# Optimization experiments

Hardware: AMD Instinct MI355X
Metric: run time of the kernel (lower is better)

The kernel has to match this reference:

```python
import jax, jax.numpy as jnp
import numpy as np

B, N, C = 2, 2048, 768
H, HD = 12, 64
HID = 3072
LN_EPS = 1e-5
POL_EPS = 1e-6


def _layer_norm(x, g, b):
    m = jnp.mean(x, axis=-1, keepdims=True)
    v = jnp.mean(jnp.square(x - m), axis=-1, keepdims=True)
    return (x - m) * jax.lax.rsqrt(v + LN_EPS) * g + b


def _softmax_with_policy(attn, policy):
    # attn: [B,H,N,N], policy: [B,N,1]
    n = attn.shape[-1]
    ap = policy.reshape(policy.shape[0], 1, 1, n)  # [B,1,1,N]
    eye = jnp.eye(n, dtype=ap.dtype)[None, None]   # [1,1,N,N]
    ap = ap + (1.0 - ap) * eye                     # always attend to self
    attn = attn - jnp.max(attn, axis=-1, keepdims=True)
    attn = jnp.exp(attn.astype(jnp.float32)) * ap.astype(jnp.float32)
    attn = (attn + POL_EPS / n) / (jnp.sum(attn, axis=-1, keepdims=True) + POL_EPS)
    return attn


def setup_inputs() -> dict:
    key = jax.random.key(0)
    ks = jax.random.split(key, 12)
    s = lambda fan_in: 1.0 / np.sqrt(fan_in)
    x = jax.random.normal(ks[0], (B, N, C), dtype=jnp.float32)
    policy = (jax.random.uniform(ks[1], (B, N, 1)) > 0.5).astype(jnp.float32)
    return {
        "x": x,
        "policy": policy,
        "ln1_g": jnp.ones((C,), jnp.float32),
        "ln1_b": jnp.zeros((C,), jnp.float32),
        "qkv_w": jax.random.uniform(ks[2], (3 * H * HD, C), jnp.float32, -s(C), s(C)),
        "proj_w": jax.random.uniform(ks[3], (C, H * HD), jnp.float32, -s(H * HD), s(H * HD)),
        "proj_b": jnp.zeros((C,), jnp.float32),
        "ln2_g": jnp.ones((C,), jnp.float32),
        "ln2_b": jnp.zeros((C,), jnp.float32),
        "fc1_w": jax.random.uniform(ks[4], (HID, C), jnp.float32, -s(C), s(C)),
        "fc1_b": jnp.zeros((HID,), jnp.float32),
        "fc2_w": jax.random.uniform(ks[5], (C, HID), jnp.float32, -s(HID), s(HID)),
        "fc2_b": jnp.zeros((C,), jnp.float32),
    }


def reference(x, policy, ln1_g, ln1_b, qkv_w, proj_w, proj_b, ln2_g, ln2_b, fc1_w, fc1_b, fc2_w, fc2_b):
    b, n, c = x.shape
    scale = HD ** -0.5
    # --- attention branch (pre-LN) ---
    h = _layer_norm(x, ln1_g, ln1_b)
    qkv = (h @ qkv_w.T).reshape(b, n, 3, H, HD).transpose(2, 0, 3, 1, 4)  # [3,B,H,N,hd]
    q, k, v = qkv[0], qkv[1], qkv[2]
    attn = jnp.einsum("bhqd,bhkd->bhqk", q * scale, k)
    attn = _softmax_with_policy(attn, policy).astype(x.dtype)
    o = jnp.einsum("bhqk,bhkd->bhqd", attn, v).transpose(0, 2, 1, 3).reshape(b, n, H * HD)
    x = x + (o @ proj_w.T + proj_b)  # skip_lam = 1.0, dropout/drop_path = identity
    # --- MLP branch (pre-LN) ---
    h = _layer_norm(x, ln2_g, ln2_b)
    h = jax.nn.gelu(h @ fc1_w.T + fc1_b, approximate=False)  # torch nn.GELU = exact erf
    x = x + (h @ fc2_w.T + fc2_b)
    return x
```

## Files before the change

kernel.cpp:

```cpp
#include <hip/hip_runtime.h>

typedef unsigned short u16;
typedef unsigned int u32;
typedef float f32x4 __attribute__((ext_vector_type(4)));
typedef float f32x16 __attribute__((ext_vector_type(16)));
typedef __bf16 bf16x8 __attribute__((ext_vector_type(8)));
typedef u16 u16x4v __attribute__((ext_vector_type(4)));
typedef u32 u32x2 __attribute__((ext_vector_type(2)));
typedef u32 u32x4 __attribute__((ext_vector_type(4)));

#define NHEAD 12
#define NN 2048
#define CC 768

#define GLOBAL_AS __attribute__((address_space(1)))
#define LDS_AS __attribute__((address_space(3)))

__device__ __forceinline__ u16 tobf(float f) {
  __bf16 h = (__bf16)f;
  return __builtin_bit_cast(u16, h);
}
__device__ __forceinline__ float bf2f(u16 h) {
  u32 u = ((u32)h) << 16;
  return __builtin_bit_cast(float, u);
}
__device__ __forceinline__ u32 cvtpk(float lo, float hi) {
  u32 r;
  asm("v_cvt_pk_bf16_f32 %0, %1, %2" : "=v"(r) : "v"(lo), "v"(hi));
  return r;
}
__device__ __forceinline__ void plswap(u32& a, u32& b) {
  asm volatile("v_permlane32_swap_b32 %0, %1" : "+v"(a), "+v"(b));
}
__device__ __forceinline__ void plswapf(float& a, float& b) {
  asm volatile("v_permlane32_swap_b32 %0, %1" : "+v"(a), "+v"(b));
}

#define N4_QKV 442368
#define N4_PROJ 147456
#define N4_FC 589824
__global__ __launch_bounds__(256) void cvt4_kernel(
    const float* __restrict__ a, const float* __restrict__ b,
    const float* __restrict__ c, const float* __restrict__ d,
    u16* __restrict__ oa, u16* __restrict__ ob, u16* __restrict__ oc,
    u16* __restrict__ od) {
  int i = blockIdx.x * 256 + threadIdx.x;
  const float* src;
  u16* dst;
  if (i < N4_QKV) {
    src = a; dst = oa;
  } else if (i < N4_QKV + N4_PROJ) {
    i -= N4_QKV; src = b; dst = ob;
  } else if (i < N4_QKV + N4_PROJ + N4_FC) {
    i -= N4_QKV + N4_PROJ; src = c; dst = oc;
  } else {
    i -= N4_QKV + N4_PROJ + N4_FC; src = d; dst = od;
    if (i >= N4_FC) return;
  }
  float4 v = ((const float4*)src)[i];
  u16x4v o = {tobf(v.x), tobf(v.y), tobf(v.z), tobf(v.w)};
  ((u16x4v*)dst)[i] = o;
}

__global__ __launch_bounds__(256) void ln_kernel(const float* __restrict__ x,
                                                 const float* __restrict__ gw,
                                                 const float* __restrict__ bw,
                                                 u16* __restrict__ out) {
  int row = blockIdx.x * 4 + (threadIdx.x >> 6);
  int lane = threadIdx.x & 63;
  const float* xr = x + (size_t)row * CC + lane * 12;
  float v[12];
  *(float4*)&v[0] = *(const float4*)(xr + 0);
  *(float4*)&v[4] = *(const float4*)(xr + 4);
  *(float4*)&v[8] = *(const float4*)(xr + 8);
  float s = 0.f, sq = 0.f;
#pragma unroll
  for (int j = 0; j < 12; ++j) { s += v[j]; sq += v[j] * v[j]; }
#pragma unroll
  for (int o = 1; o < 64; o <<= 1) { s += __shfl_xor(s, o); sq += __shfl_xor(sq, o); }
  float mean = s * (1.f / CC);
  float var = sq * (1.f / CC) - mean * mean;
  float rs = rsqrtf(var + 1e-5f);
  u16 ob[12];
#pragma unroll
  for (int j = 0; j < 12; ++j) {
    int c = lane * 12 + j;
    ob[j] = tobf((v[j] - mean) * rs * gw[c] + bw[c]);
  }
  u32* orow = (u32*)(out + (size_t)row * CC + lane * 12);
#pragma unroll
  for (int j = 0; j < 6; ++j) orow[j] = (u32)ob[2 * j] | ((u32)ob[2 * j + 1] << 16);
}

template <int BM, int OB, int HASB, int ACT, int RES>
__global__ __launch_bounds__(256) void gemm_kernel(
    const u16* __restrict__ A, const u16* __restrict__ Bw,
    const float* __restrict__ bias, const float* __restrict__ res,
    void* __restrict__ Cout, int M, int N, int K) {
  constexpr int MW = BM / 2;
  constexpr int MF = MW / 16;
  __shared__ __align__(16) u16 Alds[BM * 64];
  __shared__ __align__(16) u16 Blds[128 * 64];
  const int tid = threadIdx.x;
  const int lane = tid & 63, wave = tid >> 6;
  const int l15 = lane & 15, g = lane >> 4;
  const int nx = gridDim.x;
  const int flat = blockIdx.y * nx + blockIdx.x;
  const int cpx = (nx * gridDim.y) >> 3;
  const int swz = (flat & 7) * cpx + (flat >> 3);
  const int bm = (swz % nx) * BM, bn = (swz / nx) * 128;
  const int wm = (wave >> 1) * MW, wn = (wave & 1) * 64;
  f32x4 acc[MF][4] = {};

  for (int kt = 0; kt < K; kt += 64) {
#pragma unroll
    for (int i = 0; i < BM / 32; ++i) {
      int ob_ = i * 4096 + wave * 1024;
      int lb = ob_ + lane * 16;
      int row = lb >> 7;
      int cb = (lb & 127) ^ ((row & 7) << 4);
      const u16* sa = A + (size_t)(bm + row) * K + kt + (cb >> 1);
      __builtin_amdgcn_global_load_lds((const GLOBAL_AS void*)sa,
                                       (LDS_AS void*)(Alds + (ob_ >> 1)), 16, 0, 0);
    }
#pragma unroll
    for (int i = 0; i < 4; ++i) {
      int ob_ = i * 4096 + wave * 1024;
      int lb = ob_ + lane * 16;
      int row = lb >> 7;
      int cb = (lb & 127) ^ ((row & 7) << 4);
      const u16* sb = Bw + (size_t)(bn + row) * K + kt + (cb >> 1);
      __builtin_amdgcn_global_load_lds((const GLOBAL_AS void*)sb,
                                       (LDS_AS void*)(Blds + (ob_ >> 1)), 16, 0, 0);
    }
    __syncthreads();
#pragma unroll
    for (int ks = 0; ks < 2; ++ks) {
      bf16x8 af[MF], bfr[4];
#pragma unroll
      for (int mi = 0; mi < MF; ++mi) {
        int row = wm + mi * 16 + l15;
        int cb = (ks * 64 + g * 16) ^ ((row & 7) << 4);
        af[mi] = *(const bf16x8*)&Alds[row * 64 + (cb >> 1)];
      }
#pragma unroll
      for (int ni = 0; ni < 4; ++ni) {
        int row = wn + ni * 16 + l15;
        int cb = (ks * 64 + g * 16) ^ ((row & 7) << 4);
        bfr[ni] = *(const bf16x8*)&Blds[row * 64 + (cb >> 1)];
      }
#pragma unroll
      for (int mi = 0; mi < MF; ++mi)
#pragma unroll
        for (int ni = 0; ni < 4; ++ni)
          acc[mi][ni] = __builtin_amdgcn_mfma_f32_16x16x32_bf16(af[mi], bfr[ni],
                                                                acc[mi][ni], 0, 0, 0);
    }
    __syncthreads();
  }
#pragma unroll
  for (int mi = 0; mi < MF; ++mi) {
#pragma unroll
    for (int ni = 0; ni < 4; ++ni) {
      int col = bn + wn + ni * 16 + l15;
      float bs = HASB ? bias[col] : 0.f;
#pragma unroll
      for (int r = 0; r < 4; ++r) {
        int rowm = bm + wm + mi * 16 + g * 4 + r;
        float v = acc[mi][ni][r] + bs;
        if (ACT) v = 0.5f * v * (1.f + erff(v * 0.70710678118654752f));
        if (RES) v += res[(size_t)rowm * N + col];
        if (OB)
          ((u16*)Cout)[(size_t)rowm * N + col] = tobf(v);
        else
          ((float*)Cout)[(size_t)rowm * N + col] = v;
      }
    }
  }
}

__global__ __launch_bounds__(256) void vsum_kernel(const u16* __restrict__ qkv,
                                                   float* __restrict__ vs) {
  int bh = blockIdx.x, q4 = blockIdx.y;
  int b = bh / NHEAD, h = bh % NHEAD;
  int d = threadIdx.x & 63, part = threadIdx.x >> 6;
  float s = 0.f;
  for (int n = q4 * 512 + part; n < q4 * 512 + 512; n += 4)
    s += bf2f(qkv[(size_t)(b * NN + n) * 2304 + 2 * CC + h * 64 + d]);
  __shared__ float red[256];
  red[threadIdx.x] = s;
  __syncthreads();
  if (threadIdx.x < 64) {
    float t = red[threadIdx.x] + red[threadIdx.x + 64] + red[threadIdx.x + 128] +
              red[threadIdx.x + 192];
    vs[q4 * (24 * 64) + bh * 64 + threadIdx.x] = t;
  }
}

#define SCL2E 0.18033688f
#define TRRD(dst, addr, OFF) \
  asm volatile("ds_read_b64_tr_b16 %0, %1 offset:" OFF : "=v"(dst) : "v"(addr))

__global__ __launch_bounds__(256) void attn32_kernel(const u16* __restrict__ qkv,
                                                     const float* __restrict__ policy,
                                                     float* __restrict__ partO,
                                                     float* __restrict__ partlm) {
  __shared__ __align__(16) u16 Klds[2][4096];
  __shared__ __align__(16) u16 Vlds[2][4096];
  __shared__ float PolF[NN];
  __shared__ float alf[4][32];
  const int bh = blockIdx.y, b = bh / NHEAD, h = bh % NHEAD;
  const int qt = blockIdx.x >> 1, half = blockIdx.x & 1;
  const int tid = threadIdx.x, lane = tid & 63, w = tid >> 6;
  const int l31 = lane & 31, hp = lane >> 5, b4 = (lane >> 4) & 1;
  const int q0 = qt * 128 + w * 32;
  const int dv = q0 >> 6;
  const int ktd = (q0 >> 5) & 1;
  const int kv0 = half * 1024;
  const size_t adv = (size_t)64 * 2304;

  bf16x8 qf0, qf1, qf2, qf3;
  {
    const u16* qp = qkv + (size_t)(b * NN + q0 + l31) * 2304 + h * 64 + 8 * hp;
#pragma unroll
    for (int ds = 0; ds < 4; ++ds) {
      bf16x8 r = *(const bf16x8*)(qp + ds * 16);
      bf16x8 o;
#pragma unroll
      for (int j = 0; j < 8; ++j) o[j] = (__bf16)((float)r[j] * SCL2E);
      if (ds == 0) qf0 = o; else if (ds == 1) qf1 = o; else if (ds == 2) qf2 = o; else qf3 = o;
    }
  }

  const u16* ksrc[2];
  const u16* vsrcp[2];
#pragma unroll
  for (int c = 0; c < 2; ++c) {
    int lb = c * 4096 + w * 1024 + lane * 16;
    int row = lb >> 7;
    int cb = (lb & 127) ^ ((row & 7) << 4);
    ksrc[c] = qkv + (size_t)(b * NN + kv0 + row) * 2304 + CC + h * 64 + (cb >> 1);
    int idx0 = (c * 256 + w * 64 + lane) * 8;
    int s0 = idx0 & 15, jj = (idx0 >> 4) & 3, b4v = (idx0 >> 6) & 1,
        pv = (idx0 >> 7) & 1, hv = (idx0 >> 8) & 1, dtv = (idx0 >> 9) & 1,
        mkv = (idx0 >> 10) & 3;
    int key = mkv * 16 + 8 * hv + 4 * pv + jj;
    int d0 = dtv * 32 + 16 * b4v + s0;
    vsrcp[c] = qkv + (size_t)(b * NN + kv0 + key) * 2304 + 2 * CC + h * 64 + d0;
  }
  auto stage = [&](int buf) {
#pragma unroll
    for (int c = 0; c < 2; ++c) {
      __builtin_amdgcn_global_load_lds((const GLOBAL_AS void*)ksrc[c],
                                       (LDS_AS void*)&Klds[buf][c * 2048 + w * 512], 16, 0, 0);
      __builtin_amdgcn_global_load_lds((const GLOBAL_AS void*)vsrcp[c],
                                       (LDS_AS void*)&Vlds[buf][c * 2048 + w * 512], 16, 0, 0);
      ksrc[c] += adv; vsrcp[c] += adv;
    }
  };

  stage(0);
  {
    float4 p0 = *(const float4*)&policy[b * NN + tid * 8];
    float4 p1 = *(const float4*)&policy[b * NN + tid * 8 + 4];
    *(float4*)&PolF[tid * 8] = p0;
    *(float4*)&PolF[tid * 8 + 4] = p1;
  }
  __syncthreads();

  float m_cur = -3.0e38f, m_true = -3.0e38f, l_run = 0.f;
  f32x16 accd[2] = {};
  const u32 vbase = (u32)(uintptr_t)(LDS_AS u16*)&Vlds[0][0] +
                    (u32)(2 * (lane & 15) + 128 * b4 + 512 * hp);

#pragma unroll 1
  for (int t = 0; t < 16; ++t) {
    const int cur = t & 1;
    const int kvg = kv0 + t * 64;
    if (t < 15) stage(cur ^ 1);

    f32x16 sv0, sv1;
    {
      bf16x8 kf[4];
#pragma unroll
      for (int ds = 0; ds < 4; ++ds) {
        int row = l31;
        int cb = (32 * ds + 16 * hp) ^ ((row & 7) << 4);
        kf[ds] = *(const bf16x8*)((const char*)&Klds[cur][0] + row * 128 + cb);
      }
      f32x16 a = {};
      a = __builtin_amdgcn_mfma_f32_32x32x16_bf16(kf[0], qf0, a, 0, 0, 0);
      a = __builtin_amdgcn_mfma_f32_32x32x16_bf16(kf[1], qf1, a, 0, 0, 0);
      a = __builtin_amdgcn_mfma_f32_32x32x16_bf16(kf[2], qf2, a, 0, 0, 0);
      a = __builtin_amdgcn_mfma_f32_32x32x16_bf16(kf[3], qf3, a, 0, 0, 0);
      sv0 = a;
    }
    {
      bf16x8 kf[4];
#pragma unroll
      for (int ds = 0; ds < 4; ++ds) {
        int row = 32 + l31;
        int cb = (32 * ds + 16 * hp) ^ ((row & 7) << 4);
        kf[ds] = *(const bf16x8*)((const char*)&Klds[cur][0] + row * 128 + cb);
      }
      f32x16 a = {};
      a = __builtin_amdgcn_mfma_f32_32x32x16_bf16(kf[0], qf0, a, 0, 0, 0);
      a = __builtin_amdgcn_mfma_f32_32x32x16_bf16(kf[1], qf1, a, 0, 0, 0);
      a = __builtin_amdgcn_mfma_f32_32x32x16_bf16(kf[2], qf2, a, 0, 0, 0);
      a = __builtin_amdgcn_mfma_f32_32x32x16_bf16(kf[3], qf3, a, 0, 0, 0);
      sv1 = a;
    }

    u32x2 tr[4][2][2];
    {
      u32 vab = vbase + (u32)(cur * 8192);
      TRRD(tr[0][0][0], vab, "0");    TRRD(tr[0][0][1], vab, "256");
      TRRD(tr[0][1][0], vab, "1024"); TRRD(tr[0][1][1], vab, "1280");
      TRRD(tr[1][0][0], vab, "2048"); TRRD(tr[1][0][1], vab, "2304");
      TRRD(tr[1][1][0], vab, "3072"); TRRD(tr[1][1][1], vab, "3328");
      TRRD(tr[2][0][0], vab, "4096"); TRRD(tr[2][0][1], vab, "4352");
      TRRD(tr[3][0][0], vab, "6144"); TRRD(tr[3][0][1], vab, "6400");
      TRRD(tr[2][1][0], vab, "5120"); TRRD(tr[2][1][1], vab, "5376");
      TRRD(tr[3][1][0], vab, "7168"); TRRD(tr[3][1][1], vab, "7424");
    }

    float ta = fmaxf(fmaxf(sv0[0], sv0[1]), sv0[2]);
    float tb = fmaxf(fmaxf(sv0[3], sv0[4]), sv0[5]);
    float tc = fmaxf(fmaxf(sv0[6], sv0[7]), sv0[8]);
    float td = fmaxf(fmaxf(sv0[9], sv0[10]), sv0[11]);
    float te = fmaxf(fmaxf(sv0[12], sv0[13]), sv0[14]);
    float tf = fmaxf(fmaxf(sv0[15], sv1[0]), sv1[1]);
    float tg = fmaxf(fmaxf(sv1[2], sv1[3]), sv1[4]);
    float th = fmaxf(fmaxf(sv1[5], sv1[6]), sv1[7]);
    float ti = fmaxf(fmaxf(sv1[8], sv1[9]), sv1[10]);
    float tj = fmaxf(fmaxf(sv1[11], sv1[12]), sv1[13]);
    float tk = fmaxf(sv1[14], sv1[15]);
    float tmax = fmaxf(fmaxf(fmaxf(fmaxf(ta, tb), fmaxf(tc, td)),
                             fmaxf(fmaxf(te, tf), fmaxf(tg, th))),
                       fmaxf(fmaxf(ti, tj), tk));
    {
      float t1 = tmax, t2 = tmax;
      plswapf(t1, t2);
      tmax = fmaxf(t1, t2);
    }
    m_true = fmaxf(m_true, tmax);
    const bool defer = __all(tmax <= m_cur + 8.f);
    const float m_new = defer ? m_cur : fmaxf(m_cur, tmax);

    const bool isdiag = ((half * 16 + t) == dv);
    float ev[32];
#pragma unroll
    for (int kt = 0; kt < 2; ++kt) {
#pragma unroll
      for (int i = 0; i < 4; ++i) {
        float4 pq = *(const float4*)&PolF[kvg + kt * 32 + 8 * i + 4 * hp];
#pragma unroll
        for (int rq = 0; rq < 4; ++rq) {
          int r = 4 * i + rq;
          float ap = ((const float*)&pq)[rq];
          if (isdiag && kt == ktd) ap = ((8 * i + 4 * hp + rq) == l31) ? 1.f : ap;
          float sval = kt ? sv1[r] : sv0[r];
          ev[kt * 16 + r] = __builtin_amdgcn_exp2f(sval - m_new) * ap;
        }
      }
    }
    u32 wv[16];
#pragma unroll
    for (int j = 0; j < 16; ++j) wv[j] = cvtpk(ev[2 * j], ev[2 * j + 1]);
    float ps[16];
#pragma unroll
    for (int j = 0; j < 16; ++j)
      ps[j] = __builtin_bit_cast(float, wv[j] << 16) +
              __builtin_bit_cast(float, wv[j] & 0xffff0000u);
#pragma unroll
    for (int s = 8; s > 0; s >>= 1)
#pragma unroll
      for (int j = 0; j < s; ++j) ps[j] += ps[j + s];
    float psum = ps[0];
    {
      float s1 = psum, s2 = psum;
      plswapf(s1, s2);
      psum = s1 + s2;
    }
    if (!defer) {
      float alpha = __builtin_amdgcn_exp2f(m_cur - m_new);
      l_run = l_run * alpha + psum;
      m_cur = m_new;
      if (lane < 32) alf[w][lane] = alpha;
      float4 aq0 = *(const float4*)&alf[w][4 * hp];
      float4 aq1 = *(const float4*)&alf[w][8 + 4 * hp];
      float4 aq2 = *(const float4*)&alf[w][16 + 4 * hp];
      float4 aq3 = *(const float4*)&alf[w][24 + 4 * hp];
#pragma unroll
      for (int dt = 0; dt < 2; ++dt) {
#pragma unroll
        for (int rq = 0; rq < 4; ++rq) {
          accd[dt][0 + rq] *= ((const float*)&aq0)[rq];
          accd[dt][4 + rq] *= ((const float*)&aq1)[rq];
          accd[dt][8 + rq] *= ((const float*)&aq2)[rq];
          accd[dt][12 + rq] *= ((const float*)&aq3)[rq];
        }
      }
    } else {
      l_run += psum;
    }

    u32 PK[4][4];
#pragma unroll
    for (int mk = 0; mk < 4; ++mk) {
      int bw_ = 8 * (mk >> 1) + 4 * (mk & 1);
      PK[mk][0] = wv[bw_ + 0];
      PK[mk][1] = wv[bw_ + 1];
      PK[mk][2] = wv[bw_ + 2];
      PK[mk][3] = wv[bw_ + 3];
      plswap(PK[mk][2], PK[mk][0]);
      plswap(PK[mk][3], PK[mk][1]);
    }

    asm volatile("s_waitcnt lgkmcnt(0)" ::: "memory");
    __builtin_amdgcn_sched_barrier(0);

#pragma unroll
    for (int mk = 0; mk < 4; ++mk) {
      u32x4 pk4 = {PK[mk][0], PK[mk][1], PK[mk][2], PK[mk][3]};
      bf16x8 pf = __builtin_bit_cast(bf16x8, pk4);
#pragma unroll
      for (int dt = 0; dt < 2; ++dt) {
        u32x4 vv = {tr[mk][dt][0].x, tr[mk][dt][0].y, tr[mk][dt][1].x, tr[mk][dt][1].y};
        bf16x8 vf = __builtin_bit_cast(bf16x8, vv);
        accd[dt] = __builtin_amdgcn_mfma_f32_32x32x16_bf16(pf, vf, accd[dt], 0, 0, 0);
      }
    }
    __syncthreads();
  }

  float sr = __builtin_amdgcn_exp2f(m_cur - m_true);
  if (lane < 32) {
    alf[w][lane] = sr;
    float2 lm = {l_run * sr, m_true};
    *(float2*)&partlm[2 * ((size_t)(half * 24 + bh) * 2048 + q0 + lane)] = lm;
  }
  float4 sq0 = *(const float4*)&alf[w][4 * hp];
  float4 sq1 = *(const float4*)&alf[w][8 + 4 * hp];
  float4 sq2 = *(const float4*)&alf[w][16 + 4 * hp];
  float4 sq3 = *(const float4*)&alf[w][24 + 4 * hp];
  float* pb2 = partO + ((size_t)(half * 24 + bh) * 2048) * 64;
#pragma unroll
  for (int dt = 0; dt < 2; ++dt) {
#pragma unroll
    for (int i = 0; i < 4; ++i) {
      float4 sqv = (i == 0) ? sq0 : (i == 1) ? sq1 : (i == 2) ? sq2 : sq3;
#pragma unroll
      for (int rq = 0; rq < 4; ++rq) {
        int row = q0 + 8 * i + 4 * hp + rq;
        pb2[(size_t)row * 64 + dt * 32 + l31] = accd[dt][4 * i + rq] * ((const float*)&sqv)[rq];
      }
    }
  }
}

__global__ __launch_bounds__(256) void merge_kernel(const float* __restrict__ partO,
                                                    const float* __restrict__ partlm,
                                                    const float* __restrict__ vs,
                                                    u16* __restrict__ o) {
  int rr = blockIdx.x * 4 + (threadIdx.x >> 6);
  int lane = threadIdx.x & 63;
  int bh = rr >> 11, q = rr & 2047;
  int b = bh / NHEAD, h = bh % NHEAD;
  const float* O1 = partO + ((size_t)bh * 2048 + q) * 64;
  const float* O2 = partO + ((size_t)(24 + bh) * 2048 + q) * 64;
  float2 lm1 = ((const float2*)partlm)[(size_t)bh * 2048 + q];
  float2 lm2 = ((const float2*)partlm)[(size_t)(24 + bh) * 2048 + q];
  float ms = fmaxf(lm1.y, lm2.y);
  float w1 = exp2f(lm1.y - ms), w2 = exp2f(lm2.y - ms);
  float den = lm1.x * w1 + lm2.x * w2 + 1e-6f;
  float vsv = vs[bh * 64 + lane] + vs[1536 + bh * 64 + lane] +
              vs[3072 + bh * 64 + lane] + vs[4608 + bh * 64 + lane];
  float num = O1[lane] * w1 + O2[lane] * w2 + (1e-6f / 2048.f) * vsv;
  o[((size_t)(b * NN + q)) * CC + h * 64 + lane] = tobf(num / den);
}

extern "C" void kernel_launch(void* const* d_in, const int* in_sizes, int n_in,
                              void* d_out, int out_size, void* d_ws, size_t ws_size,
                              hipStream_t stream) {
  const float* x = (const float*)d_in[0];
  const float* policy = (const float*)d_in[1];
  const float* ln1g = (const float*)d_in[2];
  const float* ln1b = (const float*)d_in[3];
  const float* qkvw = (const float*)d_in[4];
  const float* projw = (const float*)d_in[5];
  const float* projb = (const float*)d_in[6];
  const float* ln2g = (const float*)d_in[7];
  const float* ln2b = (const float*)d_in[8];
  const float* fc1w = (const float*)d_in[9];
  const float* fc1b = (const float*)d_in[10];
  const float* fc2w = (const float*)d_in[11];
  const float* fc2b = (const float*)d_in[12];
  float* out = (float*)d_out;

  char* ws = (char*)d_ws;
  size_t off = 0;
  auto alloc = [&](size_t bytes) {
    void* p = ws + off;
    off = (off + bytes + 255) & ~(size_t)255;
    return p;
  };
  u16* wq = (u16*)alloc((size_t)2304 * 768 * 2);
  u16* wp = (u16*)alloc((size_t)768 * 768 * 2);
  u16* w1 = (u16*)alloc((size_t)3072 * 768 * 2);
  u16* w2 = (u16*)alloc((size_t)768 * 3072 * 2);
  u16* hbuf = (u16*)alloc((size_t)4096 * 768 * 2);
  u16* qkv = (u16*)alloc((size_t)4096 * 2304 * 2);
  u16* obuf = (u16*)alloc((size_t)4096 * 768 * 2);
  float* vs = (float*)alloc((size_t)4 * 24 * 64 * 4);
  size_t unionOff = off;
  float* partO = (float*)alloc((size_t)2 * 24 * 2048 * 64 * 4);
  float* partlm = (float*)alloc((size_t)2 * 24 * 2048 * 2 * 4);
  float* x1 = (float*)(ws + unionOff);
  u16* f1 = qkv;

  cvt4_kernel<<<6912, 256, 0, stream>>>(qkvw, projw, fc1w, fc2w, wq, wp, w1, w2);

  ln_kernel<<<1024, 256, 0, stream>>>(x, ln1g, ln1b, hbuf);
  gemm_kernel<128, 1, 0, 0, 0><<<dim3(32, 18), 256, 0, stream>>>(
      hbuf, wq, nullptr, nullptr, qkv, 4096, 2304, 768);
  vsum_kernel<<<dim3(24, 4), 256, 0, stream>>>(qkv, vs);
  attn32_kernel<<<dim3(32, 24), 256, 0, stream>>>(qkv, policy, partO, partlm);
  merge_kernel<<<12288, 256, 0, stream>>>(partO, partlm, vs, obuf);
  gemm_kernel<64, 0, 1, 0, 1><<<dim3(64, 6), 256, 0, stream>>>(
      obuf, wp, projb, x, x1, 4096, 768, 768);
  ln_kernel<<<1024, 256, 0, stream>>>(x1, ln2g, ln2b, hbuf);
  gemm_kernel<128, 1, 1, 1, 0><<<dim3(32, 24), 256, 0, stream>>>(
      hbuf, w1, fc1b, nullptr, f1, 4096, 3072, 768);
  gemm_kernel<64, 0, 1, 0, 1><<<dim3(64, 6), 256, 0, stream>>>(
      f1, w2, fc2b, x1, out, 4096, 768, 3072);
}
```

Before: 248.2 us.

## Compact keys/values to policy-active tokens and handle self-attention term in merge

Result: faster. 232.0 us (-6.6%).

```diff
diff --git a/kernel.cpp b/kernel.cpp
--- a/kernel.cpp
+++ b/kernel.cpp
@@ -197,27 +197,75 @@
   }
 }
 
+__global__ __launch_bounds__(256) void scan_kernel(const float* __restrict__ policy,
+                                                   int* __restrict__ ncbuf,
+                                                   int* __restrict__ idxbuf) {
+  int b = blockIdx.x, tid = threadIdx.x;
+  float pv[8];
+  *(float4*)&pv[0] = *(const float4*)&policy[b * NN + tid * 8];
+  *(float4*)&pv[4] = *(const float4*)&policy[b * NN + tid * 8 + 4];
+  int cnt = 0;
+#pragma unroll
+  for (int j = 0; j < 8; ++j) cnt += (pv[j] != 0.f) ? 1 : 0;
+  __shared__ int sc[256];
+  sc[tid] = cnt;
+  __syncthreads();
+  for (int off = 1; off < 256; off <<= 1) {
+    int v = sc[tid];
+    int add = (tid >= off) ? sc[tid - off] : 0;
+    __syncthreads();
+    sc[tid] = v + add;
+    __syncthreads();
+  }
+  int base = sc[tid] - cnt;
+#pragma unroll
+  for (int j = 0; j < 8; ++j) {
+    if (pv[j] != 0.f) idxbuf[b * NN + base++] = tid * 8 + j;
+  }
+  if (tid == 255) ncbuf[b] = sc[255];
+}
+
+__global__ __launch_bounds__(256) void gather_kernel(const u16* __restrict__ qkv,
+                                                     const int* __restrict__ ncbuf,
+                                                     const int* __restrict__ idxbuf,
+                                                     u16* __restrict__ ckv) {
+  int b = blockIdx.y;
+  int nc = ncbuf[b];
+  int ncp = (nc + 127) & ~127;
+  int c = blockIdx.x * 256 + threadIdx.x;
+  int j = c / 192, col = (c % 192) * 8;
+  if (j >= ncp) return;
+  uint4 val = {0, 0, 0, 0};
+  if (j < nc) {
+    int src = idxbuf[b * NN + j];
+    val = *(const uint4*)&qkv[(size_t)(b * NN + src) * 2304 + CC + col];
+  }
+  *(uint4*)&ckv[(size_t)(b * NN + j) * 1536 + col] = val;
+}
+
 #define SCL2E 0.18033688f
 #define TRRD(dst, addr, OFF) \
   asm volatile("ds_read_b64_tr_b16 %0, %1 offset:" OFF : "=v"(dst) : "v"(addr))
 
 __global__ __launch_bounds__(256) void attn32_kernel(const u16* __restrict__ qkv,
-                                                     const float* __restrict__ policy,
+                                                     const u16* __restrict__ ckv,
+                                                     const int* __restrict__ ncbuf,
                                                      float* __restrict__ partO,
                                                      float* __restrict__ partlm) {
   __shared__ __align__(16) u16 Klds[2][4096];
   __shared__ __align__(16) u16 Vlds[2][4096];
-  __shared__ float PolF[NN];
   __shared__ float alf[4][32];
   const int bh = blockIdx.y, b = bh / NHEAD, h = bh % NHEAD;
   const int qt = blockIdx.x >> 1, half = blockIdx.x & 1;
   const int tid = threadIdx.x, lane = tid & 63, w = tid >> 6;
   const int l31 = lane & 31, hp = lane >> 5, b4 = (lane >> 4) & 1;
   const int q0 = qt * 128 + w * 32;
-  const int dv = q0 >> 6;
-  const int ktd = (q0 >> 5) & 1;
-  const int kv0 = half * 1024;
-  const size_t adv = (size_t)64 * 2304;
+  const int nc = ncbuf[b];
+  const int ncp = (nc + 127) & ~127;
+  const int nh = ncp >> 1;
+  const int nt = nh >> 6;
+  const int kv0 = half * nh;
+  const size_t adv = (size_t)64 * 1536;
 
   bf16x8 qf0, qf1, qf2, qf3;
   {
@@ -239,14 +287,14 @@
     int lb = c * 4096 + w * 1024 + lane * 16;
     int row = lb >> 7;
     int cb = (lb & 127) ^ ((row & 7) << 4);
-    ksrc[c] = qkv + (size_t)(b * NN + kv0 + row) * 2304 + CC + h * 64 + (cb >> 1);
+    ksrc[c] = ckv + (size_t)(b * NN + kv0 + row) * 1536 + h * 64 + (cb >> 1);
     int idx0 = (c * 256 + w * 64 + lane) * 8;
     int s0 = idx0 & 15, jj = (idx0 >> 4) & 3, b4v = (idx0 >> 6) & 1,
         pv = (idx0 >> 7) & 1, hv = (idx0 >> 8) & 1, dtv = (idx0 >> 9) & 1,
         mkv = (idx0 >> 10) & 3;
     int key = mkv * 16 + 8 * hv + 4 * pv + jj;
     int d0 = dtv * 32 + 16 * b4v + s0;
-    vsrcp[c] = qkv + (size_t)(b * NN + kv0 + key) * 2304 + 2 * CC + h * 64 + d0;
+    vsrcp[c] = ckv + (size_t)(b * NN + kv0 + key) * 1536 + CC + h * 64 + d0;
   }
   auto stage = [&](int buf) {
 #pragma unroll
@@ -260,12 +308,6 @@
   };
 
   stage(0);
-  {
-    float4 p0 = *(const float4*)&policy[b * NN + tid * 8];
-    float4 p1 = *(const float4*)&policy[b * NN + tid * 8 + 4];
-    *(float4*)&PolF[tid * 8] = p0;
-    *(float4*)&PolF[tid * 8 + 4] = p1;
-  }
   __syncthreads();
 
   float m_cur = -3.0e38f, m_true = -3.0e38f, l_run = 0.f;
@@ -274,10 +316,9 @@
                     (u32)(2 * (lane & 15) + 128 * b4 + 512 * hp);
 
 #pragma unroll 1
-  for (int t = 0; t < 16; ++t) {
+  for (int t = 0; t < nt; ++t) {
     const int cur = t & 1;
-    const int kvg = kv0 + t * 64;
-    if (t < 15) stage(cur ^ 1);
+    if (t < nt - 1) stage(cur ^ 1);
 
     f32x16 sv0, sv1;
     {
@@ -347,20 +388,19 @@
     const bool defer = __all(tmax <= m_cur + 8.f);
     const float m_new = defer ? m_cur : fmaxf(m_cur, tmax);
 
-    const bool isdiag = ((half * 16 + t) == dv);
+    const int thr = nc - (kv0 + t * 64);
     float ev[32];
 #pragma unroll
     for (int kt = 0; kt < 2; ++kt) {
 #pragma unroll
       for (int i = 0; i < 4; ++i) {
-        float4 pq = *(const float4*)&PolF[kvg + kt * 32 + 8 * i + 4 * hp];
 #pragma unroll
         for (int rq = 0; rq < 4; ++rq) {
           int r = 4 * i + rq;
-          float ap = ((const float*)&pq)[rq];
-          if (isdiag && kt == ktd) ap = ((8 * i + 4 * hp + rq) == l31) ? 1.f : ap;
+          int kidx = kt * 32 + 8 * i + 4 * hp + rq;
           float sval = kt ? sv1[r] : sv0[r];
-          ev[kt * 16 + r] = __builtin_amdgcn_exp2f(sval - m_new) * ap;
+          float e = __builtin_amdgcn_exp2f(sval - m_new);
+          ev[kt * 16 + r] = (kidx < thr) ? e : 0.f;
         }
       }
     }
@@ -462,6 +502,8 @@
 __global__ __launch_bounds__(256) void merge_kernel(const float* __restrict__ partO,
                                                     const float* __restrict__ partlm,
                                                     const float* __restrict__ vs,
+                                                    const float* __restrict__ policy,
+                                                    const u16* __restrict__ qkv,
                                                     u16* __restrict__ o) {
   int rr = blockIdx.x * 4 + (threadIdx.x >> 6);
   int lane = threadIdx.x & 63;
@@ -473,10 +515,23 @@
   float2 lm2 = ((const float2*)partlm)[(size_t)(24 + bh) * 2048 + q];
   float ms = fmaxf(lm1.y, lm2.y);
   float w1 = exp2f(lm1.y - ms), w2 = exp2f(lm2.y - ms);
-  float den = lm1.x * w1 + lm2.x * w2 + 1e-6f;
+  float num_d = 0.f, den_d = 0.f;
+  if (policy[b * NN + q] == 0.f) {
+    const u16* rowp = qkv + (size_t)(b * NN + q) * 2304 + h * 64 + lane;
+    float qd = bf2f(rowp[0]);
+    float kd = bf2f(rowp[CC]);
+    float vv = bf2f(rowp[2 * CC]);
+    float dp = qd * kd;
+#pragma unroll
+    for (int of = 1; of < 64; of <<= 1) dp += __shfl_xor(dp, of);
+    float e = exp2f(dp * 0.18033688f - ms);
+    num_d = e * vv;
+    den_d = e;
+  }
+  float den = lm1.x * w1 + lm2.x * w2 + den_d + 1e-6f;
   float vsv = vs[bh * 64 + lane] + vs[1536 + bh * 64 + lane] +
               vs[3072 + bh * 64 + lane] + vs[4608 + bh * 64 + lane];
-  float num = O1[lane] * w1 + O2[lane] * w2 + (1e-6f / 2048.f) * vsv;
+  float num = O1[lane] * w1 + O2[lane] * w2 + num_d + (1e-6f / 2048.f) * vsv;
   o[((size_t)(b * NN + q)) * CC + h * 64 + lane] = tobf(num / den);
 }
 
@@ -510,14 +565,17 @@
   u16* w1 = (u16*)alloc((size_t)3072 * 768 * 2);
   u16* w2 = (u16*)alloc((size_t)768 * 3072 * 2);
   u16* hbuf = (u16*)alloc((size_t)4096 * 768 * 2);
+  u16* obuf = (u16*)alloc((size_t)4096 * 768 * 2);
   u16* qkv = (u16*)alloc((size_t)4096 * 2304 * 2);
-  u16* obuf = (u16*)alloc((size_t)4096 * 768 * 2);
   float* vs = (float*)alloc((size_t)4 * 24 * 64 * 4);
+  int* ncbuf = (int*)alloc(2 * sizeof(int));
+  int* idxbuf = (int*)alloc((size_t)2 * NN * sizeof(int));
   size_t unionOff = off;
   float* partO = (float*)alloc((size_t)2 * 24 * 2048 * 64 * 4);
   float* partlm = (float*)alloc((size_t)2 * 24 * 2048 * 2 * 4);
   float* x1 = (float*)(ws + unionOff);
-  u16* f1 = qkv;
+  u16* ckv = hbuf;
+  u16* f1 = obuf;
 
   cvt4_kernel<<<6912, 256, 0, stream>>>(qkvw, projw, fc1w, fc2w, wq, wp, w1, w2);
 
@@ -525,8 +583,10 @@
   gemm_kernel<128, 1, 0, 0, 0><<<dim3(32, 18), 256, 0, stream>>>(
       hbuf, wq, nullptr, nullptr, qkv, 4096, 2304, 768);
   vsum_kernel<<<dim3(24, 4), 256, 0, stream>>>(qkv, vs);
-  attn32_kernel<<<dim3(32, 24), 256, 0, stream>>>(qkv, policy, partO, partlm);
-  merge_kernel<<<12288, 256, 0, stream>>>(partO, partlm, vs, obuf);
+  scan_kernel<<<2, 256, 0, stream>>>(policy, ncbuf, idxbuf);
+  gather_kernel<<<dim3(1536, 2), 256, 0, stream>>>(qkv, ncbuf, idxbuf, ckv);
+  attn32_kernel<<<dim3(32, 24), 256, 0, stream>>>(qkv, ckv, ncbuf, partO, partlm);
+  merge_kernel<<<12288, 256, 0, stream>>>(partO, partlm, vs, policy, qkv, obuf);
   gemm_kernel<64, 0, 1, 0, 1><<<dim3(64, 6), 256, 0, stream>>>(
       obuf, wp, projb, x, x1, 4096, 768, 768);
   ln_kernel<<<1024, 256, 0, stream>>>(x1, ln2g, ln2b, hbuf);
```
